# Performance work log

Hardware: AMD Instinct MI355X
Metric: run time of the kernel (lower is better)

Reference implementation:

```python
import jax, jax.numpy as jnp
import numpy as np

RADII = {1: 0.031, 2: 0.028, 3: 0.128, 4: 0.096, 5: 0.084, 6: 0.073, 7: 0.071, 8: 0.066, 9: 0.057, 10: 0.058, 11: 0.166, 12: 0.141, 13: 0.121, 14: 0.111, 15: 0.107, 16: 0.105, 17: 0.102, 18: 0.106, 19: 0.2029, 20: 0.176, 21: 0.17, 22: 0.16, 23: 0.153, 24: 0.139, 25: 0.15, 26: 0.142, 27: 0.138, 28: 0.124, 29: 0.132, 30: 0.122, 31: 0.122, 32: 0.12, 33: 0.119, 34: 0.12, 35: 0.12, 36: 0.116, 37: 0.22, 38: 0.195, 39: 0.19, 40: 0.175, 41: 0.164, 42: 0.154, 43: 0.147, 44: 0.146, 45: 0.142, 46: 0.139, 47: 0.145, 48: 0.144, 49: 0.142, 50: 0.139, 51: 0.139, 52: 0.138, 53: 0.139, 54: 0.14, 55: 0.244, 56: 0.215, 57: 0.207, 58: 0.204, 59: 0.2029, 60: 0.2009, 61: 0.199, 62: 0.198, 63: 0.198, 64: 0.196, 65: 0.194, 66: 0.192, 67: 0.192, 68: 0.189, 69: 0.19, 70: 0.187, 71: 0.187, 72: 0.175, 73: 0.17, 74: 0.162, 75: 0.151, 76: 0.144, 77: 0.141, 78: 0.136, 79: 0.136, 80: 0.132, 81: 0.145, 82: 0.146, 83: 0.148, 84: 0.14, 85: 0.15, 86: 0.15, 87: 0.26, 88: 0.221, 89: 0.215, 90: 0.206, 91: 0.2, 92: 0.196, 93: 0.19, 94: 0.187, 95: 0.18, 96: 0.169}

N_ATOMS = 1_000_000
N_EDGES = 16_000_000
NUM_SYSTEMS = 10_000
MAX_Z = 97  # atomic numbers 1..96 valid
COULOMB = 138.9354576   # kJ/mol * nm / e^2
A_PREF = 0.8854 * 0.0529177210903  # Bohr-radius prefactor in nm


def setup_inputs() -> dict:
    key = jax.random.key(0)
    k1, k2, k3, k4 = jax.random.split(key, 4)
    local_pair_indices = jax.random.randint(k1, (2, N_EDGES), 0, N_ATOMS)
    # positive distances in nm, safely away from zero
    local_d_ij = jax.random.uniform(k2, (N_EDGES,), jnp.float32, 0.01, 0.5)
    atomic_numbers = jax.random.randint(k3, (N_ATOMS,), 1, MAX_Z)
    atomic_subsystem_indices = jnp.sort(
        jax.random.randint(k4, (N_ATOMS,), 0, NUM_SYSTEMS))
    radii_table = np.zeros(MAX_Z, dtype=np.float32)
    for z, r in RADII.items():
        radii_table[z] = r
    return {
        'local_d_ij': local_d_ij,
        'radii_table': jnp.asarray(radii_table),
        'local_pair_indices': local_pair_indices,
        'atomic_numbers': atomic_numbers,
        'atomic_subsystem_indices': atomic_subsystem_indices,
    }


def reference(local_d_ij, radii_table, local_pair_indices, atomic_numbers,
              atomic_subsystem_indices):
    idx_i = local_pair_indices[0]
    idx_j = local_pair_indices[1]
    # torch filters edges by idx_i < idx_j (data-dependent shape); here we
    # keep fixed shapes and zero masked contributions -> identical sums.
    mask = idx_i < idx_j

    zi_int = atomic_numbers[idx_i]
    zj_int = atomic_numbers[idx_j]
    zi = zi_int.astype(jnp.float32)
    zj = zj_int.astype(jnp.float32)
    ri = radii_table[zi_int]
    rj = radii_table[zj_int]

    d_ij = local_d_ij
    a = A_PREF / (zi ** 0.23 + zj ** 0.23)
    d = d_ij / a
    f = (0.1818 * jnp.exp(-3.2 * d)
         + 0.5099 * jnp.exp(-0.9423 * d)
         + 0.2802 * jnp.exp(-0.4029 * d)
         + 0.02817 * jnp.exp(-0.2016 * d))
    rsum = ri + rj
    phi = jnp.where(d_ij < rsum,
                    0.5 * (jnp.cos(jnp.pi * d_ij / rsum) + 1.0),
                    0.0)
    energy = f * phi * COULOMB * zi * zj / d_ij
    energy = jnp.where(mask, energy, 0.0)

    seg = atomic_subsystem_indices[idx_i]
    per_system = jax.ops.segment_sum(energy, seg, num_segments=NUM_SYSTEMS)
    return per_system.reshape(-1, 1)
```

## Files before the change

kernel.cpp:

```cpp
#include <hip/hip_runtime.h>


constexpr int MAXZ = 97;
constexpr int NBINS_PAD = 10240;
constexpr int NREP = 512;
constexpr int NPART = 32;
constexpr int WIN_SHIFT = 6;
constexpr int NWIN_MAX = 15632;

constexpr double LOG2E_D = 1.4426950408889634;
constexpr float A_INV = (float)(1.0 / (0.8854 * 0.0529177210903));
constexpr float C1 = (float)(-3.2    * LOG2E_D);
constexpr float C2 = (float)(-0.9423 * LOG2E_D);
constexpr float C3 = (float)(-0.4029 * LOG2E_D);
constexpr float C4 = (float)(-0.2016 * LOG2E_D);
constexpr float COUL = 138.9354576f;
constexpr float RMAX = 0.26f;

typedef int   iv4 __attribute__((ext_vector_type(4)));
typedef float fv4 __attribute__((ext_vector_type(4)));
typedef float fv2 __attribute__((ext_vector_type(2)));

__global__ void zero_kernel(float* __restrict__ out, int n) {
    int i = blockIdx.x * blockDim.x + threadIdx.x;
    if (i < n) out[i] = 0.0f;
}

__global__ void pack16_kernel(const int* __restrict__ z,
                              const int* __restrict__ seg,
                              unsigned short* __restrict__ p16,
                              unsigned short* __restrict__ segb, int n) {
    int i = blockIdx.x * blockDim.x + threadIdx.x;
    if (i < n) {
        int s = seg[i];
        int base = seg[(i >> WIN_SHIFT) << WIN_SHIFT];
        p16[i] = (unsigned short)((unsigned)z[i] | ((unsigned)(s - base) << 7));
        if ((i & ((1 << WIN_SHIFT) - 1)) == 0)
            segb[i >> WIN_SHIFT] = (unsigned short)s;
    }
}

__global__ void pack_kernel(const int* __restrict__ z,
                            const int* __restrict__ seg,
                            unsigned int* __restrict__ packed, int n) {
    int i = blockIdx.x * blockDim.x + threadIdx.x;
    if (i < n)
        packed[i] = (unsigned int)z[i] | ((unsigned int)seg[i] << 8);
}

__device__ __forceinline__ float zbl_energy(int zi, int zj, float d,
                                            const fv2* s_rz, bool& pass) {
    fv2 rzi = s_rz[zi];
    fv2 rzj = s_rz[zj];
    float rsum = rzi.x + rzj.x;
    pass = (d < rsum);
    float dA = d * (rzi.y + rzj.y) * A_INV;
    float f = 0.1818f  * __builtin_exp2f(C1 * dA)
            + 0.5099f  * __builtin_exp2f(C2 * dA)
            + 0.2802f  * __builtin_exp2f(C3 * dA)
            + 0.02817f * __builtin_exp2f(C4 * dA);
    float tt = d * __builtin_amdgcn_rcpf(rsum);
    float phi = 0.5f * (__builtin_amdgcn_cosf(0.5f * tt) + 1.0f);
    return f * phi * (COUL * (float)zi * (float)zj) * __builtin_amdgcn_rcpf(d);
}


__global__ __launch_bounds__(1024)
void zbl_hist_kernel(const float* __restrict__ d_ij,
                     const float* __restrict__ radii,
                     const int* __restrict__ idx_i,
                     const int* __restrict__ idx_j,
                     const unsigned short* __restrict__ p16,
                     const unsigned short* __restrict__ segb_g,
                     int nwin,
                     float* __restrict__ rep,
                     int n_edges) {
    __shared__ float s_hist[NBINS_PAD];
    __shared__ fv2 s_rz[128];
    __shared__ unsigned short s_segb[NWIN_MAX];
    const int t = threadIdx.x;

    for (int b = t; b < NBINS_PAD; b += 1024) s_hist[b] = 0.0f;
    for (int b = t; b < nwin; b += 1024) s_segb[b] = segb_g[b];
    if (t < 128) {
        fv2 v;
        v.x = (t < MAXZ) ? radii[t] : 0.0f;
        v.y = __builtin_exp2f(0.23f * __builtin_log2f((float)t));
        s_rz[t] = v;
    }
    __syncthreads();

    const int ngrp = n_edges >> 3;
    const int stride = gridDim.x * blockDim.x;
    for (int g = blockIdx.x * blockDim.x + t; g < ngrp; g += stride) {
        const iv4* pii = reinterpret_cast<const iv4*>(idx_i) + 2 * g;
        const iv4* pjj = reinterpret_cast<const iv4*>(idx_j) + 2 * g;
        const fv4* pdd = reinterpret_cast<const fv4*>(d_ij) + 2 * g;
        iv4 ii0 = __builtin_nontemporal_load(pii);
        iv4 ii1 = __builtin_nontemporal_load(pii + 1);
        iv4 jj0 = __builtin_nontemporal_load(pjj);
        iv4 jj1 = __builtin_nontemporal_load(pjj + 1);
        fv4 dd0 = __builtin_nontemporal_load(pdd);
        fv4 dd1 = __builtin_nontemporal_load(pdd + 1);

        int ia[8], ja[8];
        float da[8];
#pragma unroll
        for (int k = 0; k < 4; ++k) {
            ia[k] = ii0[k]; ia[4 + k] = ii1[k];
            ja[k] = jj0[k]; ja[4 + k] = jj1[k];
            da[k] = dd0[k]; da[4 + k] = dd1[k];
        }

        unsigned int pia[8];
        bool m[8];
#pragma unroll
        for (int k = 0; k < 8; ++k) {
            m[k] = ia[k] < ja[k];
            pia[k] = p16[m[k] ? ia[k] : 0];
        }

        bool need[8];
        unsigned int pja[8];
#pragma unroll
        for (int k = 0; k < 8; ++k) {
            int zi = (int)(pia[k] & 127u);
            float ri = s_rz[zi].x;
            need[k] = m[k] && (da[k] < ri + RMAX);
            pja[k] = p16[need[k] ? ja[k] : 0];
        }

#pragma unroll
        for (int k = 0; k < 8; ++k) {
            if (need[k]) {
                int zi = (int)(pia[k] & 127u);
                int zj = (int)(pja[k] & 127u);
                bool pass;
                float e = zbl_energy(zi, zj, da[k], s_rz, pass);
                if (pass) {
                    int seg = (int)s_segb[ia[k] >> WIN_SHIFT]
                            + (int)(pia[k] >> 7);
                    atomicAdd(&s_hist[seg], e);
                }
            }
        }
    }

    if (blockIdx.x == 0 && t == 0) {
        for (int e = ngrp << 3; e < n_edges; ++e) {
            int i = idx_i[e], j = idx_j[e];
            if (i < j) {
                unsigned int pi = p16[i], pj = p16[j];
                bool pass;
                float en = zbl_energy((int)(pi & 127u), (int)(pj & 127u),
                                      d_ij[e], s_rz, pass);
                if (pass) {
                    int seg = (int)segb_g[i >> WIN_SHIFT] + (int)(pi >> 7);
                    atomicAdd(&s_hist[seg], en);
                }
            }
        }
    }

    __syncthreads();
    fv4* __restrict__ rp =
        reinterpret_cast<fv4*>(rep + (size_t)blockIdx.x * NBINS_PAD);
    const fv4* sh = reinterpret_cast<const fv4*>(s_hist);
    for (int q = t; q < NBINS_PAD / 4; q += 1024)
        rp[q] = sh[q];
}

__global__ __launch_bounds__(256)
void reduce_all_kernel(const float* __restrict__ rep,
                       float* __restrict__ out, int out_size) {
    int bin = blockIdx.x * 256 + threadIdx.x;
    const float* p = rep + bin;
    float a0 = 0.f, a1 = 0.f, a2 = 0.f, a3 = 0.f;
    float a4 = 0.f, a5 = 0.f, a6 = 0.f, a7 = 0.f;
    for (int r = 0; r < NREP; r += 8) {
        a0 += p[(size_t)(r + 0) * NBINS_PAD];
        a1 += p[(size_t)(r + 1) * NBINS_PAD];
        a2 += p[(size_t)(r + 2) * NBINS_PAD];
        a3 += p[(size_t)(r + 3) * NBINS_PAD];
        a4 += p[(size_t)(r + 4) * NBINS_PAD];
        a5 += p[(size_t)(r + 5) * NBINS_PAD];
        a6 += p[(size_t)(r + 6) * NBINS_PAD];
        a7 += p[(size_t)(r + 7) * NBINS_PAD];
    }
    float s = ((a0 + a1) + (a2 + a3)) + ((a4 + a5) + (a6 + a7));
    if (bin < out_size) out[bin] = s;
}


template <bool PACKED>
__global__ __launch_bounds__(256)
void zbl_atomic_kernel(const float* __restrict__ d_ij,
                       const float* __restrict__ radii,
                       const int* __restrict__ idx_i,
                       const int* __restrict__ idx_j,
                       const unsigned int* __restrict__ packed,
                       const int* __restrict__ atomz,
                       const int* __restrict__ subsys,
                       float* __restrict__ out,
                       int nchunk) {
    __shared__ fv2 s_rz[128];
    int t = threadIdx.x;
    if (t < 128) {
        fv2 v;
        v.x = (t < MAXZ) ? radii[t] : 0.0f;
        v.y = __builtin_exp2f(0.23f * __builtin_log2f((float)t));
        s_rz[t] = v;
    }
    __syncthreads();

    int chunk = blockIdx.x * blockDim.x + threadIdx.x;
    if (chunk >= nchunk) return;

    iv4 ii = reinterpret_cast<const iv4*>(idx_i)[chunk];
    iv4 jj = reinterpret_cast<const iv4*>(idx_j)[chunk];
    fv4 dd = reinterpret_cast<const fv4*>(d_ij)[chunk];

#pragma unroll
    for (int k = 0; k < 4; ++k) {
        int i = ii[k];
        int j = jj[k];
        float d = dd[k];
        if (i < j) {
            int zi, zj, seg;
            if (PACKED) {
                unsigned int pi = packed[i];
                unsigned int pj = packed[j];
                zi = (int)(pi & 0xFFu);
                zj = (int)(pj & 0xFFu);
                seg = (int)(pi >> 8);
            } else {
                zi = atomz[i];
                zj = atomz[j];
                seg = subsys[i];
            }
            bool pass;
            float e = zbl_energy(zi, zj, d, s_rz, pass);
            if (pass) atomicAdd(out + seg, e);
        }
    }
}

extern "C" void kernel_launch(void* const* d_in, const int* in_sizes, int n_in,
                              void* d_out, int out_size, void* d_ws, size_t ws_size,
                              hipStream_t stream) {
    const float* d_ij  = (const float*)d_in[0];
    const float* radii = (const float*)d_in[1];
    const int* pairs   = (const int*)d_in[2];
    const int* atomz   = (const int*)d_in[3];
    const int* subsys  = (const int*)d_in[4];
    float* out = (float*)d_out;

    const int n_edges = in_sizes[2] / 2;
    const int n_atoms = in_sizes[3];
    const int* idx_i = pairs;
    const int* idx_j = pairs + n_edges;

    const int nwin = (n_atoms + (1 << WIN_SHIFT) - 1) >> WIN_SHIFT;
    const size_t p16_bytes  = ((size_t)n_atoms * 2 + 255) & ~(size_t)255;
    const size_t segb_bytes = ((size_t)nwin * 2 + 255) & ~(size_t)255;
    const size_t rep_bytes  = (size_t)NREP * NBINS_PAD * sizeof(float);
    const size_t packed_bytes = (size_t)n_atoms * sizeof(unsigned int);

    if (nwin <= NWIN_MAX &&
        ws_size >= p16_bytes + segb_bytes + rep_bytes) {
        unsigned short* p16  = (unsigned short*)d_ws;
        unsigned short* segb = (unsigned short*)((char*)d_ws + p16_bytes);
        float* rep = (float*)((char*)d_ws + p16_bytes + segb_bytes);

        pack16_kernel<<<(n_atoms + 255) / 256, 256, 0, stream>>>(
            atomz, subsys, p16, segb, n_atoms);
        zbl_hist_kernel<<<NREP, 1024, 0, stream>>>(
            d_ij, radii, idx_i, idx_j, p16, segb, nwin, rep, n_edges);
        reduce_all_kernel<<<NBINS_PAD / 256, 256, 0, stream>>>(
            rep, out, out_size);
    } else {
        zero_kernel<<<(out_size + 255) / 256, 256, 0, stream>>>(out, out_size);
        const int nchunk = n_edges / 4;
        const int blocks = (nchunk + 255) / 256;
        if (ws_size >= packed_bytes) {
            unsigned int* packed = (unsigned int*)d_ws;
            pack_kernel<<<(n_atoms + 255) / 256, 256, 0, stream>>>(
                atomz, subsys, packed, n_atoms);
            zbl_atomic_kernel<true><<<blocks, 256, 0, stream>>>(
                d_ij, radii, idx_i, idx_j, packed, atomz, subsys, out, nchunk);
        } else {
            zbl_atomic_kernel<false><<<blocks, 256, 0, stream>>>(
                d_ij, radii, idx_i, idx_j, nullptr, atomz, subsys, out, nchunk);
        }
    }
}
```

Before: 320.9 us.

## Split replica reduction into two-stage parallel reduction across many blocks

Replaces the single reduction kernel, which used 40 blocks each summing 512 replicas per bin, with a two-pass reduction. The first pass spreads the replicas over 32 partitions on a 2D grid and writes partial sums to extra workspace. The second pass sums the 32 partials per bin. This exposes more memory-level parallelism for the 20 MB replica read, at the cost of an extra launch and a larger workspace requirement.

Result: faster. 300.7 us (-6.3%).

```diff
diff --git a/kernel.cpp b/kernel.cpp
--- a/kernel.cpp
+++ b/kernel.cpp
@@ -171,24 +171,26 @@
 }
 
 __global__ __launch_bounds__(256)
-void reduce_all_kernel(const float* __restrict__ rep,
-                       float* __restrict__ out, int out_size) {
+void reduce1_kernel(const float* __restrict__ rep,
+                    float* __restrict__ partial) {
     int bin = blockIdx.x * 256 + threadIdx.x;
-    const float* p = rep + bin;
-    float a0 = 0.f, a1 = 0.f, a2 = 0.f, a3 = 0.f;
-    float a4 = 0.f, a5 = 0.f, a6 = 0.f, a7 = 0.f;
-    for (int r = 0; r < NREP; r += 8) {
-        a0 += p[(size_t)(r + 0) * NBINS_PAD];
-        a1 += p[(size_t)(r + 1) * NBINS_PAD];
-        a2 += p[(size_t)(r + 2) * NBINS_PAD];
-        a3 += p[(size_t)(r + 3) * NBINS_PAD];
-        a4 += p[(size_t)(r + 4) * NBINS_PAD];
-        a5 += p[(size_t)(r + 5) * NBINS_PAD];
-        a6 += p[(size_t)(r + 6) * NBINS_PAD];
-        a7 += p[(size_t)(r + 7) * NBINS_PAD];
-    }
-    float s = ((a0 + a1) + (a2 + a3)) + ((a4 + a5) + (a6 + a7));
-    if (bin < out_size) out[bin] = s;
+    int s = blockIdx.y;
+    float acc = 0.0f;
+    for (int r = s; r < NREP; r += NPART)
+        acc += rep[(size_t)r * NBINS_PAD + bin];
+    partial[(size_t)s * NBINS_PAD + bin] = acc;
+}
+
+__global__ __launch_bounds__(256)
+void reduce2_kernel(const float* __restrict__ partial,
+                    float* __restrict__ out, int out_size) {
+    int bin = blockIdx.x * 256 + threadIdx.x;
+    if (bin < out_size) {
+        float acc = 0.0f;
+        for (int s = 0; s < NPART; ++s)
+            acc += partial[(size_t)s * NBINS_PAD + bin];
+        out[bin] = acc;
+    }
 }
 
 
@@ -264,20 +266,25 @@
     const size_t p16_bytes  = ((size_t)n_atoms * 2 + 255) & ~(size_t)255;
     const size_t segb_bytes = ((size_t)nwin * 2 + 255) & ~(size_t)255;
     const size_t rep_bytes  = (size_t)NREP * NBINS_PAD * sizeof(float);
+    const size_t part_bytes = (size_t)NPART * NBINS_PAD * sizeof(float);
     const size_t packed_bytes = (size_t)n_atoms * sizeof(unsigned int);
 
     if (nwin <= NWIN_MAX &&
-        ws_size >= p16_bytes + segb_bytes + rep_bytes) {
+        ws_size >= p16_bytes + segb_bytes + rep_bytes + part_bytes) {
         unsigned short* p16  = (unsigned short*)d_ws;
         unsigned short* segb = (unsigned short*)((char*)d_ws + p16_bytes);
         float* rep = (float*)((char*)d_ws + p16_bytes + segb_bytes);
+        float* partial = (float*)((char*)d_ws + p16_bytes + segb_bytes +
+                                  rep_bytes);
 
         pack16_kernel<<<(n_atoms + 255) / 256, 256, 0, stream>>>(
             atomz, subsys, p16, segb, n_atoms);
         zbl_hist_kernel<<<NREP, 1024, 0, stream>>>(
             d_ij, radii, idx_i, idx_j, p16, segb, nwin, rep, n_edges);
-        reduce_all_kernel<<<NBINS_PAD / 256, 256, 0, stream>>>(
-            rep, out, out_size);
+        dim3 g1(NBINS_PAD / 256, NPART);
+        reduce1_kernel<<<g1, 256, 0, stream>>>(rep, partial);
+        reduce2_kernel<<<(out_size + 255) / 256, 256, 0, stream>>>(
+            partial, out, out_size);
     } else {
         zero_kernel<<<(out_size + 255) / 256, 256, 0, stream>>>(out, out_size);
         const int nchunk = n_edges / 4;
```
